# Performance work log

Hardware: AMD Instinct MI355X
Metric: run time of the kernel (lower is better)

## Reference

```python
import jax, jax.numpy as jnp
import numpy as np

MUL = 32          # multiplicity of 0e and 1o in node/edge/out irreps
SQRT3 = np.sqrt(3.0).astype(np.float32)


def _split(x, mul):
    # x: [E, mul + mul*3] laid out as [mul x 0e | mul x 1o]
    s = x[:, :mul]
    v = x[:, mul:].reshape(x.shape[0], mul, 3)
    return s, v


def _mlp(x, W1, W2, W3):
    # e3nn-style FullyConnectedNet: no bias, 1/sqrt(fan_in) scaling, silu between layers
    h = jax.nn.silu(x @ (W1 / np.sqrt(np.float32(W1.shape[0]))))
    h = jax.nn.silu(h @ (W2 / np.sqrt(np.float32(W2.shape[0]))))
    return h @ (W3 / np.sqrt(np.float32(W3.shape[0])))


def _tp(s1, v1, s2, v2, W1, W2, W3, W4):
    # 'uvw' tensor product with irreps2 = 1x0e+1x1o (mul2 = 1).
    # CG paths: 0e*0e->0e, 0e*1o->1o, 1o*0e->1o, 1o*1o->0e (dot/sqrt(3)).
    alpha = 1.0 / np.sqrt(np.float32(s1.shape[1]))  # path norm 1/sqrt(mul1*mul2)
    out0a = jnp.einsum('uw,eu->ew', W1, s1 * s2[:, None]) * alpha
    out1a = jnp.einsum('uw,eu,em->ewm', W2, s1, v2) * alpha
    out1b = jnp.einsum('uw,eum->ewm', W3, v1 * s2[:, None, None]) * alpha
    dot = jnp.einsum('eum,em->eu', v1, v2) / SQRT3
    out0b = jnp.einsum('uw,eu->ew', W4, dot) * alpha
    # mid irreps (sorted+simplified): [2*MUL x 0e | 2*MUL x 1o]
    return jnp.concatenate([out0a, out0b], 1), jnp.concatenate([out1a, out1b], 1)


def _lin_scale(ms, mv, w):
    # LinearScaleWithWeights: per-edge generated weights, block per irrep
    E, U = ms.shape
    ws = w[:, :U * MUL].reshape(E, U, MUL)
    wv = w[:, U * MUL:].reshape(E, U, MUL)
    a = 1.0 / np.sqrt(np.float32(U))
    return (jnp.einsum('eu,euw->ew', ms, ws) * a,
            jnp.einsum('eum,euw->ewm', mv, wv) * a)


def _lin_out(s, v, Ls, Lv):
    # o3.Linear with internal shared weights, block-diagonal per irrep
    a = 1.0 / np.sqrt(np.float32(MUL))
    return s @ Ls * a, jnp.einsum('eum,uw->ewm', v, Lv) * a


def reference(node_feats_src, node_feats_dst, edge_feats, local_env_edge, edge_scalars,
              Wn_tp1, Wn_tp2, Wn_tp3, Wn_tp4, We_tp1, We_tp2, We_tp3, We_tp4,
              Wn_mlp1, Wn_mlp2, Wn_mlp3, We_mlp1, We_mlp2, We_mlp3,
              Lns, Lnv, Les, Lev):
    ss, sv = _split(node_feats_src, MUL)
    ds, dv = _split(node_feats_dst, MUL)
    # AttentionHeadsToVector over stacked (src, dst): concat heads along mul axis
    ns = jnp.concatenate([ss, ds], 1)     # [E, 64] (64x0e)
    nv = jnp.concatenate([sv, dv], 1)     # [E, 64, 3] (64x1o)
    es, ev = _split(edge_feats, MUL)
    ls = local_env_edge[:, 0]             # 1x0e
    lv = local_env_edge[:, 1:4]           # 1x1o
    # node branch
    wn = _mlp(edge_scalars, Wn_mlp1, Wn_mlp2, Wn_mlp3)   # [E, 4096]
    ms, mv = _tp(ns, nv, ls, lv, Wn_tp1, Wn_tp2, Wn_tp3, Wn_tp4)
    n_s, n_v = _lin_scale(ms, mv, wn)
    n_s, n_v = _lin_out(n_s, n_v, Lns, Lnv)
    # edge branch
    we = _mlp(edge_scalars, We_mlp1, We_mlp2, We_mlp3)   # [E, 4096]
    ms2, mv2 = _tp(es, ev, ls, lv, We_tp1, We_tp2, We_tp3, We_tp4)
    e_s, e_v = _lin_scale(ms2, mv2, we)
    e_s, e_v = _lin_out(e_s, e_v, Les, Lev)
    out_s = n_s + e_s
    out_v = n_v + e_v
    return jnp.concatenate([out_s, out_v.reshape(out_v.shape[0], -1)], 1)  # [E, 128]


def setup_inputs() -> dict:
    key = jax.random.key(0)
    ks = jax.random.split(key, 23)
    E = 30000
    rn = lambda k, shape: jax.random.normal(k, shape, dtype=jnp.float32)
    return {
        'node_feats_src': rn(ks[0], (E, 128)),
        'node_feats_dst': rn(ks[1], (E, 128)),
        'edge_feats': rn(ks[2], (E, 128)),
        'local_env_edge': rn(ks[3], (E, 4)),
        'edge_scalars': rn(ks[4], (E, 8)),
        'Wn_tp1': rn(ks[5], (64, 32)), 'Wn_tp2': rn(ks[6], (64, 32)),
        'Wn_tp3': rn(ks[7], (64, 32)), 'Wn_tp4': rn(ks[8], (64, 32)),
        'We_tp1': rn(ks[9], (32, 32)), 'We_tp2': rn(ks[10], (32, 32)),
        'We_tp3': rn(ks[11], (32, 32)), 'We_tp4': rn(ks[12], (32, 32)),
        'Wn_mlp1': rn(ks[13], (8, 64)), 'Wn_mlp2': rn(ks[14], (64, 64)),
        'Wn_mlp3': rn(ks[15], (64, 4096)),
        'We_mlp1': rn(ks[16], (8, 64)), 'We_mlp2': rn(ks[17], (64, 64)),
        'We_mlp3': rn(ks[18], (64, 4096)),
        'Lns': rn(ks[19], (32, 32)), 'Lnv': rn(ks[20], (32, 32)),
        'Les': rn(ks[21], (32, 32)), 'Lev': rn(ks[22], (32, 32)),
    }
```

## Files before the change

kernel.cpp:

```cpp
#include <hip/hip_runtime.h>

typedef __attribute__((ext_vector_type(8))) __bf16 bf16x8;
typedef __attribute__((ext_vector_type(4))) float f32x4;

#define MFMA16(A,B,C) __builtin_amdgcn_mfma_f32_16x16x32_bf16(A,B,C,0,0,0)

typedef const __attribute__((address_space(1))) void* gas_ptr;
typedef __attribute__((address_space(3))) void* las_ptr;

#define BARRIER() do { asm volatile("" ::: "memory"); __builtin_amdgcn_s_barrier(); asm volatile("" ::: "memory"); } while (0)
#define WAIT_VM4() asm volatile("s_waitcnt vmcnt(4)" ::: "memory")
#define WAIT_VM0() asm volatile("s_waitcnt vmcnt(0)" ::: "memory")

#define WS_W3N 0
#define WS_W3E 262144
#define WS_TN  524288
#define WS_TE  532480
#define WS_M1N 536576
#define WS_M2N 538624
#define WS_M1E 542720
#define WS_M2E 544768
#define WS_CNT 548864

__global__ void prep_kernel(
    const float* __restrict__ Wn1, const float* __restrict__ Wn2,
    const float* __restrict__ Wn3, const float* __restrict__ Wn4,
    const float* __restrict__ We1, const float* __restrict__ We2,
    const float* __restrict__ We3, const float* __restrict__ We4,
    const float* __restrict__ Mn1, const float* __restrict__ Mn2, const float* __restrict__ Mn3,
    const float* __restrict__ Me1, const float* __restrict__ Me2, const float* __restrict__ Me3,
    const float* __restrict__ Lns, const float* __restrict__ Lnv,
    const float* __restrict__ Les, const float* __restrict__ Lev,
    __bf16* __restrict__ ws)
{
  int idx = blockIdx.x * 256 + threadIdx.x;
  const float c1 = 0.0027621359f;
  const float an = 0.125f;
  const float ae = 0.17677669529663687f;
  const float r3 = 0.5773502691896258f;
  const float m1s = 0.35355339059327373f;
  const float m2s = 0.125f;
  if (idx < 524288) {
    int br = idx >> 18;
    int rem = idx & 262143;
    int j = rem >> 12;
    int kc = rem & 4095;
    int vh = kc >> 11;
    int r2 = kc & 2047;
    int u = r2 >> 5, wp = r2 & 31;
    const float* M3 = br ? Me3 : Mn3;
    const float* L  = vh ? (br ? Lev : Lnv) : (br ? Les : Lns);
    const float* mrow = M3 + (size_t)j * 4096 + vh * 2048 + u * 32;
    float s = 0.f;
    #pragma unroll
    for (int w = 0; w < 32; ++w) s += mrow[w] * L[w * 32 + wp];
    ws[(br ? WS_W3E : WS_W3N) + (size_t)kc * 64 + j] = (__bf16)(s * c1);
  } else if (idx < 524288 + 8192) {
    int t = idx - 524288;
    int i = t >> 11; int r = t & 2047; int w = r >> 6; int u = r & 63;
    const float* W = (i == 0) ? Wn1 : (i == 1) ? Wn2 : (i == 2) ? Wn3 : Wn4;
    float sc = an * ((i == 3) ? r3 : 1.f);
    ws[WS_TN + t] = (__bf16)(W[u * 32 + w] * sc);
  } else if (idx < 524288 + 12288) {
    int t = idx - 532480;
    int i = t >> 10; int r = t & 1023; int w = r >> 5; int u = r & 31;
    const float* W = (i == 0) ? We1 : (i == 1) ? We2 : (i == 2) ? We3 : We4;
    float sc = ae * ((i == 3) ? r3 : 1.f);
    ws[WS_TE + t] = (__bf16)(W[u * 32 + w] * sc);
  } else if (idx < 536576 + 2048) {
    int t = idx - 536576;
    int j = t >> 5, k = t & 31;
    ws[WS_M1N + t] = (__bf16)((k < 8) ? Mn1[k * 64 + j] * m1s : 0.f);
  } else if (idx < 538624 + 4096) {
    int t = idx - 538624;
    int j2 = t >> 6, j = t & 63;
    ws[WS_M2N + t] = (__bf16)(Mn2[j * 64 + j2] * m2s);
  } else if (idx < 542720 + 2048) {
    int t = idx - 542720;
    int j = t >> 5, k = t & 31;
    ws[WS_M1E + t] = (__bf16)((k < 8) ? Me1[k * 64 + j] * m1s : 0.f);
  } else if (idx < 544768 + 4096) {
    int t = idx - 544768;
    int j2 = t >> 6, j = t & 63;
    ws[WS_M2E + t] = (__bf16)(Me2[j * 64 + j2] * m2s);
  }
}

__device__ __forceinline__ float siluf(float x) { return x / (1.0f + __expf(-x)); }
__device__ __forceinline__ unsigned int pk2(float lo, float hi) {
  unsigned short a = __builtin_bit_cast(unsigned short, (__bf16)lo);
  unsigned short b = __builtin_bit_cast(unsigned short, (__bf16)hi);
  return (unsigned int)a | ((unsigned int)b << 16);
}
__device__ __forceinline__ float bflo(unsigned int v) { return __builtin_bit_cast(float, (unsigned int)(v << 16)); }
__device__ __forceinline__ float bfhi(unsigned int v) { return __builtin_bit_cast(float, (unsigned int)(v & 0xffff0000u)); }

__global__ __launch_bounds__(256, 2) void fused_kernel(
    const float* __restrict__ nsrc, const float* __restrict__ ndst,
    const float* __restrict__ efeat, const float* __restrict__ lenv,
    const float* __restrict__ escal,
    const __bf16* __restrict__ ws,
    float* __restrict__ out, int E)
{
  __shared__ __align__(16) char lds[81920];
  const int tid = threadIdx.x;
  const int wave = tid >> 6, l = tid & 63;
  const int lg = l >> 4, li = l & 15;
  const int ebase = blockIdx.x * 64;

  char* coeff = lds;
  char* afpriv = lds + 32768 + wave * 12288;
  char* h2n = lds + 32768;
  char* h2e = lds + 32768 + 8192;

  const int uh  = wave >> 1;
  const int rtw = wave & 1;

  auto stage = [&](int buf, int branch, int b) {
    const char* gbase = (const char*)(ws + (branch ? WS_W3E : WS_W3N));
    int u = uh * 32 + b;
    char* dst = afpriv + buf * 4096 + l * 16;
    int srow = rtw * 16 + (l >> 3);
    int scol = ((l & 7) ^ (l >> 3)) << 4;
    const char* src = gbase + (size_t)u * 4096 + srow * 128 + scol;
    #pragma unroll
    for (int r = 0; r < 4; ++r) {
      int gv = r >> 1, j = r & 1;
      __builtin_amdgcn_global_load_lds((gas_ptr)(src + gv * 262144 + j * 1024),
                                       (las_ptr)(dst + gv * 2048 + j * 1024), 16, 0, 0);
    }
  };

  {
    const int br = wave >> 1;
    const __bf16* M1 = ws + (br ? WS_M1E : WS_M1N);
    const __bf16* M2 = ws + (br ? WS_M2E : WS_M2N);
    char* h2buf = br ? h2e : h2n;
    char* h1s = lds + wave * 8192;
    #pragma unroll 1
    for (int c2 = 0; c2 < 2; ++c2) {
      int ct = (wave & 1) * 2 + c2;
      int el = ct * 16 + li;
      int hl = c2 * 16 + li;
      int ee = min(ebase + el, E - 1);
      bf16x8 bx;
      #pragma unroll
      for (int i = 0; i < 8; ++i) bx[i] = (__bf16)0.f;
      if (lg == 0) {
        const float* xp = escal + (size_t)ee * 8;
        float4 t0 = *(const float4*)(xp);
        float4 t1 = *(const float4*)(xp + 4);
        bx[0]=(__bf16)t0.x; bx[1]=(__bf16)t0.y; bx[2]=(__bf16)t0.z; bx[3]=(__bf16)t0.w;
        bx[4]=(__bf16)t1.x; bx[5]=(__bf16)t1.y; bx[6]=(__bf16)t1.z; bx[7]=(__bf16)t1.w;
      }
      f32x4 hc[4];
      #pragma unroll
      for (int rt = 0; rt < 4; ++rt) {
        bf16x8 a = *(const bf16x8*)(M1 + (rt * 16 + li) * 32 + lg * 8);
        f32x4 c = {0.f, 0.f, 0.f, 0.f};
        hc[rt] = MFMA16(a, bx, c);
      }
      #pragma unroll
      for (int rt = 0; rt < 4; ++rt) {
        int j0 = rt * 16 + lg * 4;
        int g = j0 >> 3;
        int addr = hl * 128 + (((g ^ (hl & 7)) << 4)) + (j0 & 7) * 2;
        uint2 wv; wv.x = pk2(siluf(hc[rt][0]), siluf(hc[rt][1]));
        wv.y = pk2(siluf(hc[rt][2]), siluf(hc[rt][3]));
        *(uint2*)(h1s + addr) = wv;
      }
      f32x4 h2c[4];
      #pragma unroll
      for (int rt = 0; rt < 4; ++rt) { f32x4 z = {0.f,0.f,0.f,0.f}; h2c[rt] = z; }
      #pragma unroll
      for (int kj = 0; kj < 2; ++kj) {
        bf16x8 b = *(const bf16x8*)(h1s + hl * 128 + (((kj * 4 + lg) ^ (hl & 7)) << 4));
        #pragma unroll
        for (int rt = 0; rt < 4; ++rt) {
          bf16x8 a = *(const bf16x8*)(M2 + (rt * 16 + li) * 64 + kj * 32 + lg * 8);
          h2c[rt] = MFMA16(a, b, h2c[rt]);
        }
      }
      #pragma unroll
      for (int rt = 0; rt < 4; ++rt) {
        int j0 = rt * 16 + lg * 4;
        int g = j0 >> 3;
        int addr = el * 128 + (((g ^ (el & 7)) << 4)) + (j0 & 7) * 2;
        uint2 wv; wv.x = pk2(siluf(h2c[rt][0]), siluf(h2c[rt][1]));
        wv.y = pk2(siluf(h2c[rt][2]), siluf(h2c[rt][3]));
        *(uint2*)(h2buf + addr) = wv;
      }
    }
  }
  __syncthreads();

  bf16x8 bbN[4][2], bbE[4][2];
  #pragma unroll
  for (int ct = 0; ct < 4; ++ct)
    #pragma unroll
    for (int kj = 0; kj < 2; ++kj) {
      int el = ct * 16 + li;
      int off = el * 128 + (((kj * 4 + lg) ^ (el & 7)) << 4);
      bbN[ct][kj] = *(const bf16x8*)(h2n + off);
      bbE[ct][kj] = *(const bf16x8*)(h2e + off);
    }
  __syncthreads();

  auto q_phase = [&](const float* f0, const float* f1, int nk, const __bf16* T, int ustride) {
    #pragma unroll 1
    for (int ct = 0; ct < 4; ++ct) {
      int el = ct * 16 + li;
      int ee = min(ebase + el, E - 1);
      const float4 le = *(const float4*)(lenv + (size_t)ee * 4);
      const size_t erow = (size_t)ee * 128;
      if (uh == 0) {
        f32x4 q1c = {0.f,0.f,0.f,0.f}, q2c = {0.f,0.f,0.f,0.f};
        for (int kj = 0; kj < nk; ++kj) {
          const float* fp = (kj ? f1 : f0) + erow + lg * 8;
          float4 t0 = *(const float4*)(fp);
          float4 t1 = *(const float4*)(fp + 4);
          bf16x8 b;
          b[0]=(__bf16)t0.x; b[1]=(__bf16)t0.y; b[2]=(__bf16)t0.z; b[3]=(__bf16)t0.w;
          b[4]=(__bf16)t1.x; b[5]=(__bf16)t1.y; b[6]=(__bf16)t1.z; b[7]=(__bf16)t1.w;
          bf16x8 a1 = *(const bf16x8*)(T + (rtw * 16 + li) * ustride + kj * 32 + lg * 8);
          bf16x8 a2 = *(const bf16x8*)(T + 32 * ustride + (rtw * 16 + li) * ustride + kj * 32 + lg * 8);
          q1c = MFMA16(a1, b, q1c);
          q2c = MFMA16(a2, b, q2c);
        }
        #pragma unroll
        for (int r = 0; r < 4; ++r) {
          uint2 cw;
          cw.x = pk2(q1c[r] * le.x, q2c[r] * le.y);
          cw.y = pk2(q2c[r] * le.z, q2c[r] * le.w);
          *(uint2*)(coeff + (rtw * 16 + lg * 4 + r) * 512 + el * 8) = cw;
        }
      } else {
        f32x4 q30 = {0.f,0.f,0.f,0.f}, q31 = {0.f,0.f,0.f,0.f}, q32 = {0.f,0.f,0.f,0.f}, q4c = {0.f,0.f,0.f,0.f};
        for (int kj = 0; kj < nk; ++kj) {
          const float* fp = (kj ? f1 : f0) + erow + 32 + lg * 24;
          float v[24];
          #pragma unroll
          for (int q = 0; q < 6; ++q) {
            float4 t = *(const float4*)(fp + q * 4);
            v[q*4] = t.x; v[q*4+1] = t.y; v[q*4+2] = t.z; v[q*4+3] = t.w;
          }
          bf16x8 b0, b1, b2, bd;
          #pragma unroll
          for (int i = 0; i < 8; ++i) {
            b0[i] = (__bf16)v[3*i]; b1[i] = (__bf16)v[3*i+1]; b2[i] = (__bf16)v[3*i+2];
            bd[i] = (__bf16)(v[3*i] * le.y + v[3*i+1] * le.z + v[3*i+2] * le.w);
          }
          bf16x8 a3 = *(const bf16x8*)(T + 2 * 32 * ustride + (rtw * 16 + li) * ustride + kj * 32 + lg * 8);
          bf16x8 a4 = *(const bf16x8*)(T + 3 * 32 * ustride + (rtw * 16 + li) * ustride + kj * 32 + lg * 8);
          q30 = MFMA16(a3, b0, q30); q31 = MFMA16(a3, b1, q31); q32 = MFMA16(a3, b2, q32);
          q4c = MFMA16(a4, bd, q4c);
        }
        #pragma unroll
        for (int r = 0; r < 4; ++r) {
          uint2 cw;
          cw.x = pk2(q4c[r], q30[r] * le.x);
          cw.y = pk2(q31[r] * le.x, q32[r] * le.x);
          *(uint2*)(coeff + (32 + rtw * 16 + lg * 4 + r) * 512 + el * 8) = cw;
        }
      }
    }
  };

  f32x4 aS[4], aV[4][3];
  #pragma unroll
  for (int ct = 0; ct < 4; ++ct) {
    f32x4 z = {0.f,0.f,0.f,0.f};
    aS[ct] = z; aV[ct][0] = z; aV[ct][1] = z; aV[ct][2] = z;
  }

  auto main_block = [&](int buf, int b, const bf16x8 (&bb)[4][2]) {
    const char* afb = afpriv + buf * 4096;
    int u_rel = uh * 32 + b;
    bf16x8 afS[2], afV[2];
    #pragma unroll
    for (int kj = 0; kj < 2; ++kj) {
      int off = li * 128 + (((kj * 4 + lg) ^ (li & 7)) << 4);
      afS[kj] = *(const bf16x8*)(afb + off);
      afV[kj] = *(const bf16x8*)(afb + 2048 + off);
    }
    #pragma unroll
    for (int ct = 0; ct < 4; ++ct) {
      uint2 cf = *(const uint2*)(coeff + u_rel * 512 + (ct * 16 + li) * 8);
      float ms = bflo(cf.x), m0 = bfhi(cf.x), m1 = bflo(cf.y), m2 = bfhi(cf.y);
      f32x4 c = {0.f,0.f,0.f,0.f};
      c = MFMA16(afS[0], bb[ct][0], c);
      c = MFMA16(afS[1], bb[ct][1], c);
      aS[ct] += ms * c;
      f32x4 d = {0.f,0.f,0.f,0.f};
      d = MFMA16(afV[0], bb[ct][0], d);
      d = MFMA16(afV[1], bb[ct][1], d);
      aV[ct][0] += m0 * d;
      aV[ct][1] += m1 * d;
      aV[ct][2] += m2 * d;
    }
  };

  stage(0, 0, 0);
  stage(1, 0, 1);
  q_phase(nsrc, ndst, 2, ws + WS_TN, 64);
  __syncthreads();

  #pragma unroll 1
  for (int b = 0; b < 32; ++b) {
    if (b < 30) stage((b + 2) % 3, 0, b + 2);
    else        stage((b + 2) % 3, 1, b - 30);
    main_block(b % 3, b, bbN);
    WAIT_VM4();
  }
  BARRIER();

  q_phase(efeat, efeat, 1, ws + WS_TE, 32);
  __syncthreads();

  #pragma unroll 1
  for (int b = 0; b < 32; ++b) {
    if (b < 30) stage((b + 4) % 3, 1, b + 2);
    main_block((b + 2) % 3, b, bbE);
    if (b == 30) { WAIT_VM0(); }
    else         { WAIT_VM4(); }
  }
  BARRIER();

  char* R1 = lds;
  auto rmw = [&](bool add) {
    #pragma unroll
    for (int ct = 0; ct < 4; ++ct) {
      int e = ct * 16 + li;
      char* epp = R1 + e * 512;
      f32x4 s = aS[ct];
      char* p = epp + (((rtw * 4 + lg) ^ (e & 7)) << 4);
      if (add) s += *(const f32x4*)p;
      *(f32x4*)p = s;
      #pragma unroll
      for (int m = 0; m < 3; ++m) {
        f32x4 x = aV[ct][m];
        char* q = epp + (((8 + m * 8 + rtw * 4 + lg) ^ (e & 7)) << 4);
        if (add) x += *(const f32x4*)q;
        *(f32x4*)q = x;
      }
    }
  };
  if (uh == 0) rmw(false);
  __syncthreads();
  if (uh == 1) rmw(true);
  __syncthreads();

  #pragma unroll
  for (int it = 0; it < 8; ++it) {
    int chunk = it * 256 + tid;
    int e = chunk >> 5, c4 = chunk & 31;
    f32x4 v;
    #pragma unroll
    for (int q = 0; q < 4; ++q) {
      int f = c4 * 4 + q;
      int g, wd;
      if (f < 32) { g = f >> 2; wd = f & 3; }
      else { int t = f - 32; int w = t / 3; int m = t - w * 3; g = 8 + m * 8 + (w >> 2); wd = w & 3; }
      v[q] = *(const float*)(R1 + e * 512 + ((g ^ (e & 7)) << 4) + wd * 4);
    }
    int ge = ebase + e;
    if (ge < E) *(f32x4*)(out + (size_t)ge * 128 + c4 * 4) = v;
  }
}

extern "C" void kernel_launch(void* const* d_in, const int* in_sizes, int n_in,
                              void* d_out, int out_size, void* d_ws, size_t ws_size,
                              hipStream_t stream) {
  const float* nsrc  = (const float*)d_in[0];
  const float* ndst  = (const float*)d_in[1];
  const float* efeat = (const float*)d_in[2];
  const float* lenv  = (const float*)d_in[3];
  const float* escal = (const float*)d_in[4];
  const float* Wn1 = (const float*)d_in[5];
  const float* Wn2 = (const float*)d_in[6];
  const float* Wn3 = (const float*)d_in[7];
  const float* Wn4 = (const float*)d_in[8];
  const float* We1 = (const float*)d_in[9];
  const float* We2 = (const float*)d_in[10];
  const float* We3 = (const float*)d_in[11];
  const float* We4 = (const float*)d_in[12];
  const float* Mn1 = (const float*)d_in[13];
  const float* Mn2 = (const float*)d_in[14];
  const float* Mn3 = (const float*)d_in[15];
  const float* Me1 = (const float*)d_in[16];
  const float* Me2 = (const float*)d_in[17];
  const float* Me3 = (const float*)d_in[18];
  const float* Lns = (const float*)d_in[19];
  const float* Lnv = (const float*)d_in[20];
  const float* Les = (const float*)d_in[21];
  const float* Lev = (const float*)d_in[22];
  (void)n_in; (void)ws_size;

  int E = in_sizes[0] / 128;
  __bf16* ws = (__bf16*)d_ws;
  float* outp = (float*)d_out;
  (void)out_size;

  int nprep = (WS_CNT + 255) / 256;
  hipLaunchKernelGGL(prep_kernel, dim3(nprep), dim3(256), 0, stream,
                     Wn1, Wn2, Wn3, Wn4, We1, We2, We3, We4,
                     Mn1, Mn2, Mn3, Me1, Me2, Me3,
                     Lns, Lnv, Les, Lev, ws);

  int nwg = (E + 63) / 64;
  hipLaunchKernelGGL(fused_kernel, dim3(nwg), dim3(256), 0, stream,
                     nsrc, ndst, efeat, lenv, escal, ws, outp, E);
}
```

Measured before the change: 75.95 us.

## Share staged W3 tiles across all waves with block-wide double buffering

Replaces the per-wave private triple-buffered W3 staging (with explicit vmcnt waits) with block-cooperative staging of four u-rows per step into shared double buffers. The work is split into four segments (branch × u-half), and q_phase is split across edge halves. The aim is to cut redundant per-wave LDS staging and raise the amount loaded per step. In exchange it adds a __syncthreads after every step, plus more segments and q_phase calls. Staging now uses only a two-deep buffer, so less memory latency is hidden.

```diff
diff --git a/kernel.cpp b/kernel.cpp
--- a/kernel.cpp
+++ b/kernel.cpp
@@ -7,10 +7,6 @@
 
 typedef const __attribute__((address_space(1))) void* gas_ptr;
 typedef __attribute__((address_space(3))) void* las_ptr;
-
-#define BARRIER() do { asm volatile("" ::: "memory"); __builtin_amdgcn_s_barrier(); asm volatile("" ::: "memory"); } while (0)
-#define WAIT_VM4() asm volatile("s_waitcnt vmcnt(4)" ::: "memory")
-#define WAIT_VM0() asm volatile("s_waitcnt vmcnt(0)" ::: "memory")
 
 #define WS_W3N 0
 #define WS_W3E 262144
@@ -109,25 +105,25 @@
   const int ebase = blockIdx.x * 64;
 
   char* coeff = lds;
-  char* afpriv = lds + 32768 + wave * 12288;
-  char* h2n = lds + 32768;
-  char* h2e = lds + 32768 + 8192;
-
-  const int uh  = wave >> 1;
+  char* afbase = lds + 16384;
+  char* h2n = afbase;
+  char* h2e = afbase + 8192;
+
+  const int uh2 = wave >> 1;
   const int rtw = wave & 1;
-
-  auto stage = [&](int buf, int branch, int b) {
-    const char* gbase = (const char*)(ws + (branch ? WS_W3E : WS_W3N));
-    int u = uh * 32 + b;
-    char* dst = afpriv + buf * 4096 + l * 16;
-    int srow = rtw * 16 + (l >> 3);
-    int scol = ((l & 7) ^ (l >> 3)) << 4;
-    const char* src = gbase + (size_t)u * 4096 + srow * 128 + scol;
-    #pragma unroll
-    for (int r = 0; r < 4; ++r) {
-      int gv = r >> 1, j = r & 1;
-      __builtin_amdgcn_global_load_lds((gas_ptr)(src + gv * 262144 + j * 1024),
-                                       (las_ptr)(dst + gv * 2048 + j * 1024), 16, 0, 0);
+  const int rt2 = wave & 1;
+  const int eh  = wave >> 1;
+
+  auto stage = [&](int buf, const char* gb, int h, int b) {
+    char* dst = afbase + buf * 32768 + tid * 16;
+    int row = tid >> 3, col = tid & 7;
+    int roff = row * 128 + ((col ^ (row & 7)) << 4);
+    #pragma unroll
+    for (int r = 0; r < 8; ++r) {
+      int k = r >> 1, gv = r & 1;
+      int u = h * 32 + b * 4 + k;
+      const char* src = gb + gv * 262144 + (size_t)u * 4096 + roff;
+      __builtin_amdgcn_global_load_lds((gas_ptr)src, (las_ptr)(dst + r * 4096), 16, 0, 0);
     }
   };
 
@@ -136,7 +132,7 @@
     const __bf16* M1 = ws + (br ? WS_M1E : WS_M1N);
     const __bf16* M2 = ws + (br ? WS_M2E : WS_M2N);
     char* h2buf = br ? h2e : h2n;
-    char* h1s = lds + wave * 8192;
+    char* h1s = lds + wave * 4096;
     #pragma unroll 1
     for (int c2 = 0; c2 < 2; ++c2) {
       int ct = (wave & 1) * 2 + c2;
@@ -206,14 +202,15 @@
     }
   __syncthreads();
 
-  auto q_phase = [&](const float* f0, const float* f1, int nk, const __bf16* T, int ustride) {
+  auto q_phase = [&](const float* f0, const float* f1, int nk, const __bf16* T,
+                     int ustride, int h) {
     #pragma unroll 1
-    for (int ct = 0; ct < 4; ++ct) {
-      int el = ct * 16 + li;
+    for (int ct = 0; ct < 2; ++ct) {
+      int el = eh * 32 + ct * 16 + li;
       int ee = min(ebase + el, E - 1);
       const float4 le = *(const float4*)(lenv + (size_t)ee * 4);
       const size_t erow = (size_t)ee * 128;
-      if (uh == 0) {
+      if (h == 0) {
         f32x4 q1c = {0.f,0.f,0.f,0.f}, q2c = {0.f,0.f,0.f,0.f};
         for (int kj = 0; kj < nk; ++kj) {
           const float* fp = (kj ? f1 : f0) + erow + lg * 8;
@@ -222,8 +219,8 @@
           bf16x8 b;
           b[0]=(__bf16)t0.x; b[1]=(__bf16)t0.y; b[2]=(__bf16)t0.z; b[3]=(__bf16)t0.w;
           b[4]=(__bf16)t1.x; b[5]=(__bf16)t1.y; b[6]=(__bf16)t1.z; b[7]=(__bf16)t1.w;
-          bf16x8 a1 = *(const bf16x8*)(T + (rtw * 16 + li) * ustride + kj * 32 + lg * 8);
-          bf16x8 a2 = *(const bf16x8*)(T + 32 * ustride + (rtw * 16 + li) * ustride + kj * 32 + lg * 8);
+          bf16x8 a1 = *(const bf16x8*)(T + (rt2 * 16 + li) * ustride + kj * 32 + lg * 8);
+          bf16x8 a2 = *(const bf16x8*)(T + 32 * ustride + (rt2 * 16 + li) * ustride + kj * 32 + lg * 8);
           q1c = MFMA16(a1, b, q1c);
           q2c = MFMA16(a2, b, q2c);
         }
@@ -232,7 +229,7 @@
           uint2 cw;
           cw.x = pk2(q1c[r] * le.x, q2c[r] * le.y);
           cw.y = pk2(q2c[r] * le.z, q2c[r] * le.w);
-          *(uint2*)(coeff + (rtw * 16 + lg * 4 + r) * 512 + el * 8) = cw;
+          *(uint2*)(coeff + (rt2 * 16 + lg * 4 + r) * 512 + el * 8) = cw;
         }
       } else {
         f32x4 q30 = {0.f,0.f,0.f,0.f}, q31 = {0.f,0.f,0.f,0.f}, q32 = {0.f,0.f,0.f,0.f}, q4c = {0.f,0.f,0.f,0.f};
@@ -250,8 +247,8 @@
             b0[i] = (__bf16)v[3*i]; b1[i] = (__bf16)v[3*i+1]; b2[i] = (__bf16)v[3*i+2];
             bd[i] = (__bf16)(v[3*i] * le.y + v[3*i+1] * le.z + v[3*i+2] * le.w);
           }
-          bf16x8 a3 = *(const bf16x8*)(T + 2 * 32 * ustride + (rtw * 16 + li) * ustride + kj * 32 + lg * 8);
-          bf16x8 a4 = *(const bf16x8*)(T + 3 * 32 * ustride + (rtw * 16 + li) * ustride + kj * 32 + lg * 8);
+          bf16x8 a3 = *(const bf16x8*)(T + 2 * 32 * ustride + (rt2 * 16 + li) * ustride + kj * 32 + lg * 8);
+          bf16x8 a4 = *(const bf16x8*)(T + 3 * 32 * ustride + (rt2 * 16 + li) * ustride + kj * 32 + lg * 8);
           q30 = MFMA16(a3, b0, q30); q31 = MFMA16(a3, b1, q31); q32 = MFMA16(a3, b2, q32);
           q4c = MFMA16(a4, bd, q4c);
         }
@@ -260,7 +257,7 @@
           uint2 cw;
           cw.x = pk2(q4c[r], q30[r] * le.x);
           cw.y = pk2(q31[r] * le.x, q32[r] * le.x);
-          *(uint2*)(coeff + (32 + rtw * 16 + lg * 4 + r) * 512 + el * 8) = cw;
+          *(uint2*)(coeff + (rt2 * 16 + lg * 4 + r) * 512 + el * 8) = cw;
         }
       }
     }
@@ -274,57 +271,54 @@
   }
 
   auto main_block = [&](int buf, int b, const bf16x8 (&bb)[4][2]) {
-    const char* afb = afpriv + buf * 4096;
-    int u_rel = uh * 32 + b;
-    bf16x8 afS[2], afV[2];
-    #pragma unroll
-    for (int kj = 0; kj < 2; ++kj) {
-      int off = li * 128 + (((kj * 4 + lg) ^ (li & 7)) << 4);
-      afS[kj] = *(const bf16x8*)(afb + off);
-      afV[kj] = *(const bf16x8*)(afb + 2048 + off);
-    }
-    #pragma unroll
-    for (int ct = 0; ct < 4; ++ct) {
-      uint2 cf = *(const uint2*)(coeff + u_rel * 512 + (ct * 16 + li) * 8);
-      float ms = bflo(cf.x), m0 = bfhi(cf.x), m1 = bflo(cf.y), m2 = bfhi(cf.y);
-      f32x4 c = {0.f,0.f,0.f,0.f};
-      c = MFMA16(afS[0], bb[ct][0], c);
-      c = MFMA16(afS[1], bb[ct][1], c);
-      aS[ct] += ms * c;
-      f32x4 d = {0.f,0.f,0.f,0.f};
-      d = MFMA16(afV[0], bb[ct][0], d);
-      d = MFMA16(afV[1], bb[ct][1], d);
-      aV[ct][0] += m0 * d;
-      aV[ct][1] += m1 * d;
-      aV[ct][2] += m2 * d;
+    #pragma unroll
+    for (int j = 0; j < 2; ++j) {
+      int k = uh2 * 2 + j;
+      int urow = b * 4 + k;
+      const char* afb = afbase + buf * 32768 + k * 8192;
+      bf16x8 afS[2], afV[2];
+      #pragma unroll
+      for (int kj = 0; kj < 2; ++kj) {
+        int off = (rtw * 16 + li) * 128 + (((kj * 4 + lg) ^ (li & 7)) << 4);
+        afS[kj] = *(const bf16x8*)(afb + off);
+        afV[kj] = *(const bf16x8*)(afb + 4096 + off);
+      }
+      #pragma unroll
+      for (int ct = 0; ct < 4; ++ct) {
+        uint2 cf = *(const uint2*)(coeff + urow * 512 + (ct * 16 + li) * 8);
+        float ms = bflo(cf.x), m0 = bfhi(cf.x), m1 = bflo(cf.y), m2 = bfhi(cf.y);
+        f32x4 c = {0.f,0.f,0.f,0.f};
+        c = MFMA16(afS[0], bb[ct][0], c);
+        c = MFMA16(afS[1], bb[ct][1], c);
+        aS[ct] += ms * c;
+        f32x4 d = {0.f,0.f,0.f,0.f};
+        d = MFMA16(afV[0], bb[ct][0], d);
+        d = MFMA16(afV[1], bb[ct][1], d);
+        aV[ct][0] += m0 * d;
+        aV[ct][1] += m1 * d;
+        aV[ct][2] += m2 * d;
+      }
     }
   };
 
-  stage(0, 0, 0);
-  stage(1, 0, 1);
-  q_phase(nsrc, ndst, 2, ws + WS_TN, 64);
-  __syncthreads();
-
-  #pragma unroll 1
-  for (int b = 0; b < 32; ++b) {
-    if (b < 30) stage((b + 2) % 3, 0, b + 2);
-    else        stage((b + 2) % 3, 1, b - 30);
-    main_block(b % 3, b, bbN);
-    WAIT_VM4();
-  }
-  BARRIER();
-
-  q_phase(efeat, efeat, 1, ws + WS_TE, 32);
-  __syncthreads();
-
-  #pragma unroll 1
-  for (int b = 0; b < 32; ++b) {
-    if (b < 30) stage((b + 4) % 3, 1, b + 2);
-    main_block((b + 2) % 3, b, bbE);
-    if (b == 30) { WAIT_VM0(); }
-    else         { WAIT_VM4(); }
-  }
-  BARRIER();
+  auto run_seg = [&](int br, int h, const bf16x8 (&bb)[4][2]) {
+    const char* gb = (const char*)(ws + (br ? WS_W3E : WS_W3N));
+    stage(0, gb, h, 0);
+    if (br == 0) q_phase(nsrc, ndst, 2, ws + WS_TN, 64, h);
+    else         q_phase(efeat, efeat, 1, ws + WS_TE, 32, h);
+    __syncthreads();
+    #pragma unroll 1
+    for (int b = 0; b < 8; ++b) {
+      if (b < 7) stage((b + 1) & 1, gb, h, b + 1);
+      main_block(b & 1, b, bb);
+      __syncthreads();
+    }
+  };
+
+  run_seg(0, 0, bbN);
+  run_seg(0, 1, bbN);
+  run_seg(1, 0, bbE);
+  run_seg(1, 1, bbE);
 
   char* R1 = lds;
   auto rmw = [&](bool add) {
@@ -345,9 +339,9 @@
       }
     }
   };
-  if (uh == 0) rmw(false);
+  if (uh2 == 0) rmw(false);
   __syncthreads();
-  if (uh == 1) rmw(true);
+  if (uh2 == 1) rmw(true);
   __syncthreads();
 
   #pragma unroll
```

After: 77.77 us. 1.02x slower.
